# Performance work log

Measured on AMD Instinct MI355X. Metric: run time of the kernel, lower is better.

The kernel has to match this reference:

```python
import jax, jax.numpy as jnp
import numpy as np

B, DIM, N, K, NA = 1, 64, 1024, 16, 12
POS_HID = 64
ATTN_HID = 4 * DIM


def setup_inputs() -> dict:
    key = jax.random.key(0)
    ks = jax.random.split(key, 8)
    s = 0.05  # small init scale, mimics xavier magnitude
    return {
        "xyz": jax.random.normal(ks[0], (B, 3, N), jnp.float32),
        "feats": jax.random.normal(ks[1], (B, DIM, N, NA), jnp.float32),
        "anchors": jax.random.normal(ks[2], (NA, 3, 3), jnp.float32),
        "to_qkv": jax.random.normal(ks[3], (3 * DIM, DIM), jnp.float32) * s,
        "pos_mlp1": jax.random.normal(ks[4], (POS_HID, 3), jnp.float32) * s,
        "pos_mlp2": jax.random.normal(ks[5], (DIM, POS_HID), jnp.float32) * s,
        "attn_mlp1": jax.random.normal(ks[6], (ATTN_HID, DIM), jnp.float32) * s,
        "attn_mlp2": jax.random.normal(ks[7], (DIM, ATTN_HID), jnp.float32) * s,
    }


def reference(xyz, feats, anchors, to_qkv, pos_mlp1, pos_mlp2, attn_mlp1, attn_mlp2):
    # --- KNN over points (self included) ---
    pts = jnp.swapaxes(xyz, 1, 2)                      # [B,N,3]
    sq = jnp.sum(pts * pts, axis=-1)                   # [B,N]
    d2 = sq[:, :, None] + sq[:, None, :] - 2.0 * jnp.einsum('bnd,bmd->bnm', pts, pts)
    _, idx = jax.lax.top_k(-d2, K)                     # [B,N,K] nearest indices

    # --- gather helpers (vmapped over batch) ---
    gather3 = jax.vmap(lambda x, i: x[:, i])           # [C,N],[N,K] -> [C,N,K]
    gather4 = jax.vmap(lambda x, i: x[:, i, :])        # [C,N,A],[N,K] -> [C,N,K,A]

    # --- relative positions rotated by anchors ---
    grouped_xyz = gather3(xyz, idx)                    # [B,3,N,K]
    rel = xyz[:, :, :, None] - grouped_xyz             # [B,3,N,K]
    gx = jnp.einsum('aij,bjnk->binka', anchors, rel)   # [B,3,N,K,NA]

    # --- positional embedding MLP ---
    pe = jnp.einsum('ji,binka->bjnka', pos_mlp1, gx)   # [B,POS_HID,N,K,NA]
    pe = jax.nn.relu(pe)
    pe = jnp.einsum('ji,binka->bjnka', pos_mlp2, pe)   # [B,DIM,N,K,NA]

    # --- qkv projection ---
    qkv = jnp.einsum('ji,bina->bjna', to_qkv, feats)   # [B,3*DIM,N,NA]
    q, k, v = jnp.split(qkv, 3, axis=1)                # each [B,DIM,N,NA]

    k_g = gather4(k, idx)                              # [B,DIM,N,K,NA]
    v_g = gather4(v, idx) + pe                         # [B,DIM,N,K,NA]
    qk_rel = q[:, :, :, None, :] - k_g                 # [B,DIM,N,K,NA]

    # --- attention MLP on (qk_rel + pe) ---
    sim = qk_rel + pe
    sim = jnp.einsum('ji,binka->bjnka', attn_mlp1, sim)  # [B,4*DIM,N,K,NA]
    sim = jax.nn.relu(sim)
    sim = jnp.einsum('ji,binka->bjnka', attn_mlp2, sim)  # [B,DIM,N,K,NA]

    # --- per-channel softmax over neighbor axis, aggregate ---
    attn = jax.nn.softmax(sim, axis=-2)
    return jnp.sum(attn * v_g, axis=-2)                # [B,DIM,N,NA]
```

## Files before the change

### kernel.cpp

```cpp
#include <hip/hip_runtime.h>

#define NPTS 1024
#define DIM 64
#define KNN 16
#define NA 12
#define NCOL 192

typedef __attribute__((ext_vector_type(8))) short bf16x8;
typedef __attribute__((ext_vector_type(4))) float f32x4;

static __device__ inline unsigned short f2bfu(float x) {
    __bf16 b = (__bf16)x;
    return __builtin_bit_cast(unsigned short, b);
}
static __device__ inline unsigned pk2(float lo, float hi) {
    return (unsigned)f2bfu(lo) | ((unsigned)f2bfu(hi) << 16);
}
static __device__ inline bf16x8 load8_cvt(const float* p) {
    f32x4 u = *(const f32x4*)p;
    f32x4 v = *(const f32x4*)(p + 4);
    bf16x8 r;
    r[0] = (short)f2bfu(u[0]); r[1] = (short)f2bfu(u[1]); r[2] = (short)f2bfu(u[2]); r[3] = (short)f2bfu(u[3]);
    r[4] = (short)f2bfu(v[0]); r[5] = (short)f2bfu(v[1]); r[6] = (short)f2bfu(v[2]); r[7] = (short)f2bfu(v[3]);
    return r;
}

__global__ __launch_bounds__(256) void qkv_kernel(const float* __restrict__ feats,
                                                  const float* __restrict__ to_qkv,
                                                  float* __restrict__ qkvT,
                                                  unsigned short* __restrict__ pack,
                                                  const float* __restrict__ pos2,
                                                  const float* __restrict__ am1,
                                                  const float* __restrict__ am2) {
    __shared__ unsigned short XT[48][72];
    const int n0 = blockIdx.x * 48;
    const int t = threadIdx.x;
    for (int e = t; e < 48 * 64; e += 256) {
        int c = e % 48, i = e / 48;
        XT[c][i] = f2bfu(feats[i * (NPTS * NA) + n0 + c]);
    }
    __syncthreads();
    const int lane = t & 63, w = t >> 6, c16 = lane & 15, g = lane >> 4;

    bf16x8 bfr[3][2];
    #pragma unroll
    for (int ni = 0; ni < 3; ++ni)
        #pragma unroll
        for (int kt = 0; kt < 2; ++kt) {
            int cd = (w * 3 + ni) * 16 + c16;
            bfr[ni][kt] = load8_cvt(to_qkv + cd * 64 + kt * 32 + g * 8);
        }

    const f32x4 zero4 = {0.f, 0.f, 0.f, 0.f};
    #pragma unroll
    for (int mt = 0; mt < 3; ++mt) {
        f32x4 acc[3] = {zero4, zero4, zero4};
        #pragma unroll
        for (int kt = 0; kt < 2; ++kt) {
            bf16x8 af = *(const bf16x8*)&XT[mt * 16 + c16][kt * 32 + g * 8];
            #pragma unroll
            for (int ni = 0; ni < 3; ++ni)
                acc[ni] = __builtin_amdgcn_mfma_f32_16x16x32_bf16(af, bfr[ni][kt], acc[ni], 0, 0, 0);
        }
        #pragma unroll
        for (int ni = 0; ni < 3; ++ni) {
            int cd = (w * 3 + ni) * 16 + c16;
            int c = cd >> 6, d = cd & 63;
            #pragma unroll
            for (int r = 0; r < 4; ++r) {
                int na = n0 + mt * 16 + 4 * g + r;
                qkvT[c * (NPTS * NA * DIM) + na * 64 + d] = acc[ni][r];
            }
        }
    }

    if (blockIdx.x < 72 && t < 64) {
        int s = blockIdx.x;
        int c16p = t & 15, gp = t >> 4;
        const float* src;
        if (s < 8) {
            int mg = s >> 1, kt = s & 1;
            src = pos2 + (mg * 16 + c16p) * 64 + kt * 32 + gp * 8;
        } else if (s < 40) {
            int u = s - 8, hq = u >> 3, mg = (u >> 1) & 3, kt = u & 1;
            src = am1 + (hq * 64 + mg * 16 + c16p) * 64 + kt * 32 + gp * 8;
        } else {
            int u = s - 40, hq = u >> 3, mg = (u >> 1) & 3, kt = u & 1;
            src = am2 + (mg * 16 + c16p) * 256 + hq * 64 + kt * 32 + gp * 8;
        }
        unsigned short* dst = pack + (s * 64 + t) * 8;
        #pragma unroll
        for (int e = 0; e < 8; ++e) dst[e] = f2bfu(src[e]);
    }
}

__global__ __launch_bounds__(256) void knn_kernel(const float* __restrict__ xyz,
                                                  int* __restrict__ idxout) {
    __shared__ float px[NPTS], py[NPTS], pz[NPTS];
    const int t = threadIdx.x;
    for (int m = t; m < NPTS; m += 256) {
        px[m] = xyz[m];
        py[m] = xyz[NPTS + m];
        pz[m] = xyz[2 * NPTS + m];
    }
    __syncthreads();
    const int lane = t & 63, w = t >> 6;
    const int n = blockIdx.x * 4 + w;
    const float xn = px[n], yn = py[n], zn = pz[n];
    const float sqn = xn * xn + yn * yn + zn * zn;
    float dd[16]; int id[16];
    #pragma unroll
    for (int j = 0; j < 16; ++j) {
        int m = j * 64 + lane;
        float xm = px[m], ym = py[m], zm = pz[m];
        float sqm = xm * xm + ym * ym + zm * zm;
        float dot = xn * xm + yn * ym + zn * zm;
        dd[j] = sqn + sqm - 2.f * dot;
        id[j] = m;
    }
    for (int r = 0; r < KNN; ++r) {
        float bd = 1e30f; int bi = 0x7fffffff;
        #pragma unroll
        for (int j = 0; j < 16; ++j)
            if (dd[j] < bd || (dd[j] == bd && id[j] < bi)) { bd = dd[j]; bi = id[j]; }
        #pragma unroll
        for (int mask = 1; mask < 64; mask <<= 1) {
            float od = __shfl_xor(bd, mask);
            int oi = __shfl_xor(bi, mask);
            if (od < bd || (od == bd && oi < bi)) { bd = od; bi = oi; }
        }
        if (lane == 0) idxout[n * KNN + r] = bi;
        #pragma unroll
        for (int j = 0; j < 16; ++j)
            if (id[j] == bi) dd[j] = 1e30f;
    }
}

__global__ __launch_bounds__(512, 4) void attn_main(const float* __restrict__ xyz,
                                                    const float* __restrict__ anchors,
                                                    const float* __restrict__ pos1,
                                                    const unsigned short* __restrict__ pack,
                                                    const float* __restrict__ qT,
                                                    const float* __restrict__ kT,
                                                    const float* __restrict__ vT,
                                                    const int* __restrict__ nn,
                                                    float* __restrict__ out) {
    __shared__ __align__(16) unsigned short XbT[NCOL][72];
    __shared__ __align__(16) unsigned short HqT[NCOL][72];
    __shared__ float relb[KNN][3];
    __shared__ float ab[108];
    __shared__ int nidx[KNN];

    const int n = blockIdx.x, t = threadIdx.x;
    const int lane = t & 63, wave = t >> 6;
    const int c16 = lane & 15, g = lane >> 4;
    const int mg = wave >> 1, ng = wave & 1;

    if (t < 108) ab[t] = anchors[t];
    if (t < KNN) {
        int m = nn[n * KNN + t];
        nidx[t] = m;
        relb[t][0] = xyz[n] - xyz[m];
        relb[t][1] = xyz[NPTS + n] - xyz[NPTS + m];
        relb[t][2] = xyz[2 * NPTS + n] - xyz[2 * NPTS + m];
    }
    __syncthreads();

    {
        const float p10 = pos1[lane * 3 + 0], p11 = pos1[lane * 3 + 1], p12 = pos1[lane * 3 + 2];
        #pragma unroll
        for (int j = 0; j < 24; ++j) {
            int c = wave + 8 * j;
            int a = c >> 4, k = c & 15;
            float rx = relb[k][0], ry = relb[k][1], rz = relb[k][2];
            float g0 = ab[a * 9 + 0] * rx + ab[a * 9 + 1] * ry + ab[a * 9 + 2] * rz;
            float g1 = ab[a * 9 + 3] * rx + ab[a * 9 + 4] * ry + ab[a * 9 + 5] * rz;
            float g2 = ab[a * 9 + 6] * rx + ab[a * 9 + 7] * ry + ab[a * 9 + 8] * rz;
            float p = p10 * g0 + p11 * g1 + p12 * g2;
            XbT[c][lane] = f2bfu(p > 0.f ? p : 0.f);
        }
    }
    __syncthreads();

    const bf16x8* pk16 = (const bf16x8*)pack;
    const f32x4 zero4 = {0.f, 0.f, 0.f, 0.f};

    f32x4 peacc[6] = {zero4, zero4, zero4, zero4, zero4, zero4};
    #pragma unroll
    for (int kt = 0; kt < 2; ++kt) {
        bf16x8 p2f = pk16[(mg * 2 + kt) * 64 + lane];
        #pragma unroll
        for (int i = 0; i < 6; ++i) {
            bf16x8 pb = *(const bf16x8*)&XbT[(ng * 6 + i) * 16 + c16][kt * 32 + g * 8];
            peacc[i] = __builtin_amdgcn_mfma_f32_16x16x32_bf16(p2f, pb, peacc[i], 0, 0, 0);
        }
    }

    float vgk[6][4], xreg[6][4];
    {
        const int m = nidx[c16];
        const int d0 = mg * 16 + 4 * g;
        #pragma unroll
        for (int i = 0; i < 6; ++i) {
            int a = ng * 6 + i;
            f32x4 qv = *(const f32x4*)&qT[(n * NA + a) * DIM + d0];
            f32x4 kg = *(const f32x4*)&kT[(m * NA + a) * DIM + d0];
            f32x4 vv = *(const f32x4*)&vT[(m * NA + a) * DIM + d0];
            #pragma unroll
            for (int r = 0; r < 4; ++r) {
                vgk[i][r] = vv[r] + peacc[i][r];
                xreg[i][r] = qv[r] - kg[r] + peacc[i][r];
            }
        }
    }
    __syncthreads();
    #pragma unroll
    for (int i = 0; i < 6; ++i) {
        int col = (ng * 6 + i) * 16 + c16;
        int row0 = mg * 16 + 4 * g;
        *(unsigned*)&XbT[col][row0]     = pk2(xreg[i][0], xreg[i][1]);
        *(unsigned*)&XbT[col][row0 + 2] = pk2(xreg[i][2], xreg[i][3]);
    }
    __syncthreads();

    f32x4 sacc[6] = {zero4, zero4, zero4, zero4, zero4, zero4};
    for (int hq = 0; hq < 4; ++hq) {
        f32x4 hacc[6] = {zero4, zero4, zero4, zero4, zero4, zero4};
        #pragma unroll
        for (int kt = 0; kt < 2; ++kt) {
            bf16x8 w1f = pk16[(8 + (hq * 4 + mg) * 2 + kt) * 64 + lane];
            #pragma unroll
            for (int i = 0; i < 6; ++i) {
                bf16x8 xb = *(const bf16x8*)&XbT[(ng * 6 + i) * 16 + c16][kt * 32 + g * 8];
                hacc[i] = __builtin_amdgcn_mfma_f32_16x16x32_bf16(w1f, xb, hacc[i], 0, 0, 0);
            }
        }
        #pragma unroll
        for (int i = 0; i < 6; ++i) {
            int col = (ng * 6 + i) * 16 + c16;
            int hrow = mg * 16 + 4 * g;
            *(unsigned*)&HqT[col][hrow]     = pk2(fmaxf(hacc[i][0], 0.f), fmaxf(hacc[i][1], 0.f));
            *(unsigned*)&HqT[col][hrow + 2] = pk2(fmaxf(hacc[i][2], 0.f), fmaxf(hacc[i][3], 0.f));
        }
        __syncthreads();
        #pragma unroll
        for (int kt = 0; kt < 2; ++kt) {
            bf16x8 w2f = pk16[(40 + (hq * 4 + mg) * 2 + kt) * 64 + lane];
            #pragma unroll
            for (int i = 0; i < 6; ++i) {
                bf16x8 hb = *(const bf16x8*)&HqT[(ng * 6 + i) * 16 + c16][kt * 32 + g * 8];
                sacc[i] = __builtin_amdgcn_mfma_f32_16x16x32_bf16(w2f, hb, sacc[i], 0, 0, 0);
            }
        }
        __syncthreads();
    }

    #pragma unroll
    for (int i = 0; i < 6; ++i) {
        int a = ng * 6 + i;
        #pragma unroll
        for (int r = 0; r < 4; ++r) {
            float e = __expf(sacc[i][r]);
            float den = e, num = e * vgk[i][r];
            #pragma unroll
            for (int mask = 1; mask < 16; mask <<= 1) {
                den += __shfl_xor(den, mask);
                num += __shfl_xor(num, mask);
            }
            if (c16 == 0) {
                int d = mg * 16 + 4 * g + r;
                out[(d * NPTS + n) * NA + a] = num / den;
            }
        }
    }
}

extern "C" void kernel_launch(void* const* d_in, const int* in_sizes, int n_in,
                              void* d_out, int out_size, void* d_ws, size_t ws_size,
                              hipStream_t stream) {
    const float* xyz     = (const float*)d_in[0];
    const float* feats   = (const float*)d_in[1];
    const float* anchors = (const float*)d_in[2];
    const float* to_qkv  = (const float*)d_in[3];
    const float* pos1    = (const float*)d_in[4];
    const float* pos2    = (const float*)d_in[5];
    const float* am1     = (const float*)d_in[6];
    const float* am2     = (const float*)d_in[7];
    float* out = (float*)d_out;

    float* ws = (float*)d_ws;
    const int seg = NPTS * NA * DIM;
    float* qT = ws;
    float* kT = ws + seg;
    float* vT = ws + 2 * seg;
    int* nn = (int*)(ws + 3 * seg);
    unsigned short* pack = (unsigned short*)(ws + 3 * seg + NPTS * KNN);

    qkv_kernel<<<256, 256, 0, stream>>>(feats, to_qkv, qT, pack, pos2, am1, am2);
    knn_kernel<<<256, 256, 0, stream>>>(xyz, nn);
    attn_main<<<NPTS, 512, 0, stream>>>(xyz, anchors, pos1, pack, qT, kT, vT, nn, out);
}
```

Baseline: 94.60 us.

## Fuse qkv and knn kernels, swap MFMA operand roles, precompute anchor-rotated offsets

Merges the qkv projection and KNN kernels into one prep launch to save a kernel launch and let the two independent workloads share blocks. In the attention kernel, points now feed the MFMA A operand and weights the B operand, so each wave owns a 2x3 tile layout and the softmax over neighbours reduces inside lane registers with only two cross-lane shuffles. It also precomputes the rotated relative positions once in shared memory and pads the shared tiles to a row stride of 76. The trade-off is that gathered k/v values are now loaded as scalars instead of float4, and transposed stores to shared memory write single bf16 values.

```diff
diff --git a/kernel.cpp b/kernel.cpp
--- a/kernel.cpp
+++ b/kernel.cpp
@@ -5,6 +5,7 @@
 #define KNN 16
 #define NA 12
 #define NCOL 192
+#define XPAD 76
 
 typedef __attribute__((ext_vector_type(8))) short bf16x8;
 typedef __attribute__((ext_vector_type(4))) float f32x4;
@@ -12,9 +13,6 @@
 static __device__ inline unsigned short f2bfu(float x) {
     __bf16 b = (__bf16)x;
     return __builtin_bit_cast(unsigned short, b);
-}
-static __device__ inline unsigned pk2(float lo, float hi) {
-    return (unsigned)f2bfu(lo) | ((unsigned)f2bfu(hi) << 16);
 }
 static __device__ inline bf16x8 load8_cvt(const float* p) {
     f32x4 u = *(const f32x4*)p;
@@ -25,114 +23,115 @@
     return r;
 }
 
-__global__ __launch_bounds__(256) void qkv_kernel(const float* __restrict__ feats,
-                                                  const float* __restrict__ to_qkv,
-                                                  float* __restrict__ qkvT,
-                                                  unsigned short* __restrict__ pack,
-                                                  const float* __restrict__ pos2,
-                                                  const float* __restrict__ am1,
-                                                  const float* __restrict__ am2) {
+__global__ __launch_bounds__(256) void prep_kernel(const float* __restrict__ feats,
+                                                   const float* __restrict__ to_qkv,
+                                                   float* __restrict__ qkvT,
+                                                   unsigned short* __restrict__ pack,
+                                                   const float* __restrict__ pos2,
+                                                   const float* __restrict__ am1,
+                                                   const float* __restrict__ am2,
+                                                   const float* __restrict__ xyz,
+                                                   int* __restrict__ idxout) {
     __shared__ unsigned short XT[48][72];
+    __shared__ float px[NPTS], py[NPTS], pz[NPTS];
+    const int t = threadIdx.x;
     const int n0 = blockIdx.x * 48;
-    const int t = threadIdx.x;
-    for (int e = t; e < 48 * 64; e += 256) {
-        int c = e % 48, i = e / 48;
-        XT[c][i] = f2bfu(feats[i * (NPTS * NA) + n0 + c]);
-    }
-    __syncthreads();
-    const int lane = t & 63, w = t >> 6, c16 = lane & 15, g = lane >> 4;
-
-    bf16x8 bfr[3][2];
-    #pragma unroll
-    for (int ni = 0; ni < 3; ++ni)
-        #pragma unroll
-        for (int kt = 0; kt < 2; ++kt) {
-            int cd = (w * 3 + ni) * 16 + c16;
-            bfr[ni][kt] = load8_cvt(to_qkv + cd * 64 + kt * 32 + g * 8);
-        }
-
-    const f32x4 zero4 = {0.f, 0.f, 0.f, 0.f};
-    #pragma unroll
-    for (int mt = 0; mt < 3; ++mt) {
-        f32x4 acc[3] = {zero4, zero4, zero4};
-        #pragma unroll
-        for (int kt = 0; kt < 2; ++kt) {
-            bf16x8 af = *(const bf16x8*)&XT[mt * 16 + c16][kt * 32 + g * 8];
-            #pragma unroll
-            for (int ni = 0; ni < 3; ++ni)
-                acc[ni] = __builtin_amdgcn_mfma_f32_16x16x32_bf16(af, bfr[ni][kt], acc[ni], 0, 0, 0);
-        }
-        #pragma unroll
-        for (int ni = 0; ni < 3; ++ni) {
-            int cd = (w * 3 + ni) * 16 + c16;
-            int c = cd >> 6, d = cd & 63;
-            #pragma unroll
-            for (int r = 0; r < 4; ++r) {
-                int na = n0 + mt * 16 + 4 * g + r;
-                qkvT[c * (NPTS * NA * DIM) + na * 64 + d] = acc[ni][r];
-            }
-        }
-    }
 
     if (blockIdx.x < 72 && t < 64) {
         int s = blockIdx.x;
         int c16p = t & 15, gp = t >> 4;
         const float* src;
         if (s < 8) {
-            int mg = s >> 1, kt = s & 1;
-            src = pos2 + (mg * 16 + c16p) * 64 + kt * 32 + gp * 8;
+            int nt = s >> 1, kt = s & 1;
+            src = pos2 + (nt * 16 + c16p) * 64 + kt * 32 + gp * 8;
         } else if (s < 40) {
-            int u = s - 8, hq = u >> 3, mg = (u >> 1) & 3, kt = u & 1;
-            src = am1 + (hq * 64 + mg * 16 + c16p) * 64 + kt * 32 + gp * 8;
+            int u = s - 8, hq = u >> 3, nt = (u >> 1) & 3, kt = u & 1;
+            src = am1 + (hq * 64 + nt * 16 + c16p) * 64 + kt * 32 + gp * 8;
         } else {
-            int u = s - 40, hq = u >> 3, mg = (u >> 1) & 3, kt = u & 1;
-            src = am2 + (mg * 16 + c16p) * 256 + hq * 64 + kt * 32 + gp * 8;
+            int u = s - 40, hq = u >> 3, nt = (u >> 1) & 3, kt = u & 1;
+            src = am2 + (nt * 16 + c16p) * 256 + hq * 64 + kt * 32 + gp * 8;
         }
         unsigned short* dst = pack + (s * 64 + t) * 8;
         #pragma unroll
         for (int e = 0; e < 8; ++e) dst[e] = f2bfu(src[e]);
     }
-}
-
-__global__ __launch_bounds__(256) void knn_kernel(const float* __restrict__ xyz,
-                                                  int* __restrict__ idxout) {
-    __shared__ float px[NPTS], py[NPTS], pz[NPTS];
-    const int t = threadIdx.x;
+
     for (int m = t; m < NPTS; m += 256) {
         px[m] = xyz[m];
         py[m] = xyz[NPTS + m];
         pz[m] = xyz[2 * NPTS + m];
     }
-    __syncthreads();
-    const int lane = t & 63, w = t >> 6;
-    const int n = blockIdx.x * 4 + w;
-    const float xn = px[n], yn = py[n], zn = pz[n];
-    const float sqn = xn * xn + yn * yn + zn * zn;
-    float dd[16]; int id[16];
-    #pragma unroll
-    for (int j = 0; j < 16; ++j) {
-        int m = j * 64 + lane;
-        float xm = px[m], ym = py[m], zm = pz[m];
-        float sqm = xm * xm + ym * ym + zm * zm;
-        float dot = xn * xm + yn * ym + zn * zm;
-        dd[j] = sqn + sqm - 2.f * dot;
-        id[j] = m;
-    }
-    for (int r = 0; r < KNN; ++r) {
-        float bd = 1e30f; int bi = 0x7fffffff;
-        #pragma unroll
-        for (int j = 0; j < 16; ++j)
-            if (dd[j] < bd || (dd[j] == bd && id[j] < bi)) { bd = dd[j]; bi = id[j]; }
-        #pragma unroll
-        for (int mask = 1; mask < 64; mask <<= 1) {
-            float od = __shfl_xor(bd, mask);
-            int oi = __shfl_xor(bi, mask);
-            if (od < bd || (od == bd && oi < bi)) { bd = od; bi = oi; }
-        }
-        if (lane == 0) idxout[n * KNN + r] = bi;
-        #pragma unroll
-        for (int j = 0; j < 16; ++j)
-            if (id[j] == bi) dd[j] = 1e30f;
+    for (int e = t; e < 48 * 64; e += 256) {
+        int c = e % 48, i = e / 48;
+        XT[c][i] = f2bfu(feats[i * (NPTS * NA) + n0 + c]);
+    }
+    __syncthreads();
+
+    const int lane = t & 63, w = t >> 6, c16 = lane & 15, g = lane >> 4;
+
+    {
+        bf16x8 bfr[3][2];
+        #pragma unroll
+        for (int ni = 0; ni < 3; ++ni)
+            #pragma unroll
+            for (int kt = 0; kt < 2; ++kt) {
+                int cd = (w * 3 + ni) * 16 + c16;
+                bfr[ni][kt] = load8_cvt(to_qkv + cd * 64 + kt * 32 + g * 8);
+            }
+        const f32x4 zero4 = {0.f, 0.f, 0.f, 0.f};
+        #pragma unroll
+        for (int mt = 0; mt < 3; ++mt) {
+            f32x4 acc[3] = {zero4, zero4, zero4};
+            #pragma unroll
+            for (int kt = 0; kt < 2; ++kt) {
+                bf16x8 af = *(const bf16x8*)&XT[mt * 16 + c16][kt * 32 + g * 8];
+                #pragma unroll
+                for (int ni = 0; ni < 3; ++ni)
+                    acc[ni] = __builtin_amdgcn_mfma_f32_16x16x32_bf16(af, bfr[ni][kt], acc[ni], 0, 0, 0);
+            }
+            #pragma unroll
+            for (int ni = 0; ni < 3; ++ni) {
+                int cd = (w * 3 + ni) * 16 + c16;
+                int c = cd >> 6, d = cd & 63;
+                #pragma unroll
+                for (int r = 0; r < 4; ++r) {
+                    int na = n0 + mt * 16 + 4 * g + r;
+                    qkvT[c * (NPTS * NA * DIM) + na * 64 + d] = acc[ni][r];
+                }
+            }
+        }
+    }
+
+    {
+        const int n = blockIdx.x * 4 + w;
+        const float xn = px[n], yn = py[n], zn = pz[n];
+        const float sqn = xn * xn + yn * yn + zn * zn;
+        float dd[16]; int id[16];
+        #pragma unroll
+        for (int j = 0; j < 16; ++j) {
+            int m = j * 64 + lane;
+            float xm = px[m], ym = py[m], zm = pz[m];
+            float sqm = xm * xm + ym * ym + zm * zm;
+            float dot = xn * xm + yn * ym + zn * zm;
+            dd[j] = sqn + sqm - 2.f * dot;
+            id[j] = m;
+        }
+        for (int r = 0; r < KNN; ++r) {
+            float bd = 1e30f; int bi = 0x7fffffff;
+            #pragma unroll
+            for (int j = 0; j < 16; ++j)
+                if (dd[j] < bd || (dd[j] == bd && id[j] < bi)) { bd = dd[j]; bi = id[j]; }
+            #pragma unroll
+            for (int mask = 1; mask < 64; mask <<= 1) {
+                float od = __shfl_xor(bd, mask);
+                int oi = __shfl_xor(bi, mask);
+                if (od < bd || (od == bd && oi < bi)) { bd = od; bi = oi; }
+            }
+            if (lane == 0) idxout[n * KNN + r] = bi;
+            #pragma unroll
+            for (int j = 0; j < 16; ++j)
+                if (id[j] == bi) dd[j] = 1e30f;
+        }
     }
 }
 
@@ -145,16 +144,18 @@
                                                     const float* __restrict__ vT,
                                                     const int* __restrict__ nn,
                                                     float* __restrict__ out) {
-    __shared__ __align__(16) unsigned short XbT[NCOL][72];
-    __shared__ __align__(16) unsigned short HqT[NCOL][72];
+    __shared__ __align__(16) unsigned short XbT[NCOL][XPAD];
+    __shared__ __align__(16) unsigned short HqT[NCOL][XPAD];
     __shared__ float relb[KNN][3];
     __shared__ float ab[108];
+    __shared__ float gbuf[3][NCOL];
     __shared__ int nidx[KNN];
 
     const int n = blockIdx.x, t = threadIdx.x;
     const int lane = t & 63, wave = t >> 6;
     const int c16 = lane & 15, g = lane >> 4;
-    const int mg = wave >> 1, ng = wave & 1;
+    const int mw = wave & 3;
+    const int nw = wave >> 2;
 
     if (t < 108) ab[t] = anchors[t];
     if (t < KNN) {
@@ -166,18 +167,22 @@
     }
     __syncthreads();
 
+    for (int e = t; e < 3 * NCOL; e += 512) {
+        int row = e / NCOL, col = e % NCOL;
+        int a = col >> 4, k = col & 15;
+        gbuf[row][col] = ab[a * 9 + row * 3 + 0] * relb[k][0]
+                       + ab[a * 9 + row * 3 + 1] * relb[k][1]
+                       + ab[a * 9 + row * 3 + 2] * relb[k][2];
+    }
+    __syncthreads();
+
     {
         const float p10 = pos1[lane * 3 + 0], p11 = pos1[lane * 3 + 1], p12 = pos1[lane * 3 + 2];
         #pragma unroll
         for (int j = 0; j < 24; ++j) {
-            int c = wave + 8 * j;
-            int a = c >> 4, k = c & 15;
-            float rx = relb[k][0], ry = relb[k][1], rz = relb[k][2];
-            float g0 = ab[a * 9 + 0] * rx + ab[a * 9 + 1] * ry + ab[a * 9 + 2] * rz;
-            float g1 = ab[a * 9 + 3] * rx + ab[a * 9 + 4] * ry + ab[a * 9 + 5] * rz;
-            float g2 = ab[a * 9 + 6] * rx + ab[a * 9 + 7] * ry + ab[a * 9 + 8] * rz;
-            float p = p10 * g0 + p11 * g1 + p12 * g2;
-            XbT[c][lane] = f2bfu(p > 0.f ? p : 0.f);
+            int col = wave + 8 * j;
+            float p = p10 * gbuf[0][col] + p11 * gbuf[1][col] + p12 * gbuf[2][col];
+            XbT[col][lane] = f2bfu(p > 0.f ? p : 0.f);
         }
     }
     __syncthreads();
@@ -188,39 +193,48 @@
     f32x4 peacc[6] = {zero4, zero4, zero4, zero4, zero4, zero4};
     #pragma unroll
     for (int kt = 0; kt < 2; ++kt) {
-        bf16x8 p2f = pk16[(mg * 2 + kt) * 64 + lane];
-        #pragma unroll
-        for (int i = 0; i < 6; ++i) {
-            bf16x8 pb = *(const bf16x8*)&XbT[(ng * 6 + i) * 16 + c16][kt * 32 + g * 8];
-            peacc[i] = __builtin_amdgcn_mfma_f32_16x16x32_bf16(p2f, pb, peacc[i], 0, 0, 0);
+        bf16x8 b0 = pk16[((2 * nw + 0) * 2 + kt) * 64 + lane];
+        bf16x8 b1 = pk16[((2 * nw + 1) * 2 + kt) * 64 + lane];
+        #pragma unroll
+        for (int mi = 0; mi < 3; ++mi) {
+            bf16x8 af = *(const bf16x8*)&XbT[(mw + 4 * mi) * 16 + c16][kt * 32 + g * 8];
+            peacc[mi * 2 + 0] = __builtin_amdgcn_mfma_f32_16x16x32_bf16(af, b0, peacc[mi * 2 + 0], 0, 0, 0);
+            peacc[mi * 2 + 1] = __builtin_amdgcn_mfma_f32_16x16x32_bf16(af, b1, peacc[mi * 2 + 1], 0, 0, 0);
         }
     }
 
     float vgk[6][4], xreg[6][4];
     {
-        const int m = nidx[c16];
-        const int d0 = mg * 16 + 4 * g;
-        #pragma unroll
-        for (int i = 0; i < 6; ++i) {
-            int a = ng * 6 + i;
-            f32x4 qv = *(const f32x4*)&qT[(n * NA + a) * DIM + d0];
-            f32x4 kg = *(const f32x4*)&kT[(m * NA + a) * DIM + d0];
-            f32x4 vv = *(const f32x4*)&vT[(m * NA + a) * DIM + d0];
-            #pragma unroll
-            for (int r = 0; r < 4; ++r) {
-                vgk[i][r] = vv[r] + peacc[i][r];
-                xreg[i][r] = qv[r] - kg[r] + peacc[i][r];
+        const int m0 = nidx[4 * g + 0], m1 = nidx[4 * g + 1];
+        const int m2 = nidx[4 * g + 2], m3 = nidx[4 * g + 3];
+        #pragma unroll
+        for (int mi = 0; mi < 3; ++mi) {
+            int a = mw + 4 * mi;
+            #pragma unroll
+            for (int ni = 0; ni < 2; ++ni) {
+                int tile = mi * 2 + ni;
+                int d = (2 * nw + ni) * 16 + c16;
+                float qv = qT[(n * NA + a) * DIM + d];
+                int b0 = (m0 * NA + a) * DIM + d, b1 = (m1 * NA + a) * DIM + d;
+                int b2 = (m2 * NA + a) * DIM + d, b3 = (m3 * NA + a) * DIM + d;
+                xreg[tile][0] = qv - kT[b0] + peacc[tile][0]; vgk[tile][0] = vT[b0] + peacc[tile][0];
+                xreg[tile][1] = qv - kT[b1] + peacc[tile][1]; vgk[tile][1] = vT[b1] + peacc[tile][1];
+                xreg[tile][2] = qv - kT[b2] + peacc[tile][2]; vgk[tile][2] = vT[b2] + peacc[tile][2];
+                xreg[tile][3] = qv - kT[b3] + peacc[tile][3]; vgk[tile][3] = vT[b3] + peacc[tile][3];
             }
         }
     }
     __syncthreads();
     #pragma unroll
-    for (int i = 0; i < 6; ++i) {
-        int col = (ng * 6 + i) * 16 + c16;
-        int row0 = mg * 16 + 4 * g;
-        *(unsigned*)&XbT[col][row0]     = pk2(xreg[i][0], xreg[i][1]);
-        *(unsigned*)&XbT[col][row0 + 2] = pk2(xreg[i][2], xreg[i][3]);
-    }
+    for (int mi = 0; mi < 3; ++mi)
+        #pragma unroll
+        for (int ni = 0; ni < 2; ++ni) {
+            int tile = mi * 2 + ni;
+            int col = (2 * nw + ni) * 16 + c16;
+            #pragma unroll
+            for (int r = 0; r < 4; ++r)
+                XbT[(mw + 4 * mi) * 16 + 4 * g + r][col] = f2bfu(xreg[tile][r]);
+        }
     __syncthreads();
 
     f32x4 sacc[6] = {zero4, zero4, zero4, zero4, zero4, zero4};
@@ -228,49 +242,57 @@
         f32x4 hacc[6] = {zero4, zero4, zero4, zero4, zero4, zero4};
         #pragma unroll
         for (int kt = 0; kt < 2; ++kt) {
-            bf16x8 w1f = pk16[(8 + (hq * 4 + mg) * 2 + kt) * 64 + lane];
-            #pragma unroll
-            for (int i = 0; i < 6; ++i) {
-                bf16x8 xb = *(const bf16x8*)&XbT[(ng * 6 + i) * 16 + c16][kt * 32 + g * 8];
-                hacc[i] = __builtin_amdgcn_mfma_f32_16x16x32_bf16(w1f, xb, hacc[i], 0, 0, 0);
-            }
-        }
-        #pragma unroll
-        for (int i = 0; i < 6; ++i) {
-            int col = (ng * 6 + i) * 16 + c16;
-            int hrow = mg * 16 + 4 * g;
-            *(unsigned*)&HqT[col][hrow]     = pk2(fmaxf(hacc[i][0], 0.f), fmaxf(hacc[i][1], 0.f));
-            *(unsigned*)&HqT[col][hrow + 2] = pk2(fmaxf(hacc[i][2], 0.f), fmaxf(hacc[i][3], 0.f));
-        }
+            bf16x8 b0 = pk16[(8 + (hq * 4 + 2 * nw + 0) * 2 + kt) * 64 + lane];
+            bf16x8 b1 = pk16[(8 + (hq * 4 + 2 * nw + 1) * 2 + kt) * 64 + lane];
+            #pragma unroll
+            for (int mi = 0; mi < 3; ++mi) {
+                bf16x8 af = *(const bf16x8*)&XbT[(mw + 4 * mi) * 16 + c16][kt * 32 + g * 8];
+                hacc[mi * 2 + 0] = __builtin_amdgcn_mfma_f32_16x16x32_bf16(af, b0, hacc[mi * 2 + 0], 0, 0, 0);
+                hacc[mi * 2 + 1] = __builtin_amdgcn_mfma_f32_16x16x32_bf16(af, b1, hacc[mi * 2 + 1], 0, 0, 0);
+            }
+        }
+        #pragma unroll
+        for (int mi = 0; mi < 3; ++mi)
+            #pragma unroll
+            for (int ni = 0; ni < 2; ++ni) {
+                int tile = mi * 2 + ni;
+                int col = (2 * nw + ni) * 16 + c16;
+                #pragma unroll
+                for (int r = 0; r < 4; ++r)
+                    HqT[(mw + 4 * mi) * 16 + 4 * g + r][col] = f2bfu(fmaxf(hacc[tile][r], 0.f));
+            }
         __syncthreads();
         #pragma unroll
         for (int kt = 0; kt < 2; ++kt) {
-            bf16x8 w2f = pk16[(40 + (hq * 4 + mg) * 2 + kt) * 64 + lane];
-            #pragma unroll
-            for (int i = 0; i < 6; ++i) {
-                bf16x8 hb = *(const bf16x8*)&HqT[(ng * 6 + i) * 16 + c16][kt * 32 + g * 8];
-                sacc[i] = __builtin_amdgcn_mfma_f32_16x16x32_bf16(w2f, hb, sacc[i], 0, 0, 0);
+            bf16x8 b0 = pk16[(40 + hq * 8 + (2 * nw + 0) * 2 + kt) * 64 + lane];
+            bf16x8 b1 = pk16[(40 + hq * 8 + (2 * nw + 1) * 2 + kt) * 64 + lane];
+            #pragma unroll
+            for (int mi = 0; mi < 3; ++mi) {
+                bf16x8 af = *(const bf16x8*)&HqT[(mw + 4 * mi) * 16 + c16][kt * 32 + g * 8];
+                sacc[mi * 2 + 0] = __builtin_amdgcn_mfma_f32_16x16x32_bf16(af, b0, sacc[mi * 2 + 0], 0, 0, 0);
+                sacc[mi * 2 + 1] = __builtin_amdgcn_mfma_f32_16x16x32_bf16(af, b1, sacc[mi * 2 + 1], 0, 0, 0);
             }
         }
         __syncthreads();
     }
 
     #pragma unroll
-    for (int i = 0; i < 6; ++i) {
-        int a = ng * 6 + i;
-        #pragma unroll
-        for (int r = 0; r < 4; ++r) {
-            float e = __expf(sacc[i][r]);
-            float den = e, num = e * vgk[i][r];
-            #pragma unroll
-            for (int mask = 1; mask < 16; mask <<= 1) {
-                den += __shfl_xor(den, mask);
-                num += __shfl_xor(num, mask);
-            }
-            if (c16 == 0) {
-                int d = mg * 16 + 4 * g + r;
+    for (int mi = 0; mi < 3; ++mi) {
+        int a = mw + 4 * mi;
+        #pragma unroll
+        for (int ni = 0; ni < 2; ++ni) {
+            int tile = mi * 2 + ni;
+            int d = (2 * nw + ni) * 16 + c16;
+            float e0 = __expf(sacc[tile][0]);
+            float e1 = __expf(sacc[tile][1]);
+            float e2 = __expf(sacc[tile][2]);
+            float e3 = __expf(sacc[tile][3]);
+            float den = (e0 + e1) + (e2 + e3);
+            float num = (e0 * vgk[tile][0] + e1 * vgk[tile][1]) + (e2 * vgk[tile][2] + e3 * vgk[tile][3]);
+            den += __shfl_xor(den, 16); num += __shfl_xor(num, 16);
+            den += __shfl_xor(den, 32); num += __shfl_xor(num, 32);
+            if (g == 0)
                 out[(d * NPTS + n) * NA + a] = num / den;
-            }
         }
     }
 }
@@ -296,7 +318,6 @@
     int* nn = (int*)(ws + 3 * seg);
     unsigned short* pack = (unsigned short*)(ws + 3 * seg + NPTS * KNN);
 
-    qkv_kernel<<<256, 256, 0, stream>>>(feats, to_qkv, qT, pack, pos2, am1, am2);
-    knn_kernel<<<256, 256, 0, stream>>>(xyz, nn);
+    prep_kernel<<<256, 256, 0, stream>>>(feats, to_qkv, qT, pack, pos2, am1, am2, xyz, nn);
     attn_main<<<NPTS, 512, 0, stream>>>(xyz, anchors, pos1, pack, qT, kT, vT, nn, out);
 }
```

New measurement: 76.54 us. 1.24x faster.
